# Kernel tuning notes

Measured on AMD Instinct MI355X. Metric: run time of the kernel, lower is better.

## Reference

```python
import jax, jax.numpy as jnp
import numpy as np

B, C, T = 64, 128, 500
N_RES, N_CLASSES = 2048, 10
DECAY_RES, DECAY_CLF = 0.9, 0.9
V_TH_RES, V_TH_CLF = 1.0, 1.0


def setup_inputs() -> dict:
    key = jax.random.key(0)
    k1, k2, k3, k4 = jax.random.split(key, 4)
    x = jax.random.normal(k1, (B, C, T), dtype=jnp.float32)
    # learned / fixed parameters sized per init_kwargs
    W_in = jax.random.normal(k2, (N_RES, C), dtype=jnp.float32) * (1.0 / np.sqrt(C))
    W_res = jax.random.normal(k3, (N_RES, N_RES), dtype=jnp.float32) * (1.0 / np.sqrt(N_RES))
    W_clf = jax.random.normal(k4, (N_CLASSES, N_RES), dtype=jnp.float32) * (1.0 / np.sqrt(N_RES))
    return {"x": x, "W_in": W_in, "W_res": W_res, "W_clf": W_clf}


def reference(x, W_in, W_res, W_clf):
    """x: (B, C, T). Returns (spike_counts (B, n_classes), reservoir_spikes_accum (B, n_reservoir)).
    LIF reservoir + single-voter LIF readout, no STDP updates (use_stdp=False path)."""
    Bb = x.shape[0]
    dtype = x.dtype

    def step(carry, x_t):  # x_t: (B, C)
        v_r, s_prev, v_c = carry
        # reservoir LIF: leak + feedforward input + recurrent spike input
        I = x_t @ W_in.T + s_prev @ W_res.T          # (B, N_RES)
        v_r = DECAY_RES * v_r + I
        s = (v_r >= V_TH_RES).astype(dtype)          # spike
        v_r = v_r * (1.0 - s)                        # reset fired neurons
        # classifier (STDPLayer forward, plasticity disabled)
        v_c = DECAY_CLF * v_c + s @ W_clf.T          # (B, N_CLASSES)
        c = (v_c >= V_TH_CLF).astype(dtype)
        v_c = v_c * (1.0 - c)
        return (v_r, s, v_c), (c, s)

    init = (jnp.zeros((Bb, N_RES), dtype),
            jnp.zeros((Bb, N_RES), dtype),
            jnp.zeros((Bb, N_CLASSES), dtype))
    xs = jnp.moveaxis(x, 2, 0)                       # (T, B, C)
    _, (clf_spikes, res_spikes) = jax.lax.scan(step, init, xs)
    spike_counts = clf_spikes.sum(axis=0)            # (B, N_CLASSES)
    reservoir_spikes_accum = res_spikes.sum(axis=0)  # (B, N_RES)
    return spike_counts, reservoir_spikes_accum
```

## Files before the change

kernel.cpp:

```cpp
#include <hip/hip_runtime.h>
#include <cstdint>
#include <cstddef>

#define B_    64
#define C_    128
#define T_    500
#define NRES  2048
#define NCLS  10

#define NWG   256
#define SL    8
#define NT    1024
#define WROW  520
#define WPIT  (4 * WROW)



#define WS_MASK0   0
#define WS_MASK1   16384
#define WS_FLAG    32768
#define WS_ARR     49152
#define WS_WORDS   13312
#define NFLAG      16
#define CHKWG      (NWG - 1)

typedef float v2f __attribute__((ext_vector_type(2)));

struct SMem {
  float    WtT2[SL][WPIT];
  float    WinT2[SL][C_];
  float    xs2[2][B_][C_ + 1];
  unsigned mask[B_][65];
  double   clfred2[2][NCLS];
};

__global__ void zero_ws_kernel(unsigned* __restrict__ p, int n) {
  int i = blockIdx.x * blockDim.x + threadIdx.x;
  if (i < n) p[i] = 0u;
}

#define ACC2(ACC, WB, M0, M1, JB) do {                                        \
  const unsigned _lo = (unsigned)(((int)((M0) << (31 - (JB)))) >> 31) & (WB); \
  const unsigned _hi = (unsigned)(((int)((M1) << (31 - (JB)))) >> 31) & (WB); \
  v2f _m; _m.x = __uint_as_float(_lo); _m.y = __uint_as_float(_hi);           \
  (ACC) = (ACC) + _m;                                                         \
} while (0)

#define BT_STEP(X, D, MLO) do {                                            \
  const unsigned _y = (unsigned)__shfl_xor((int)(X), (D), 64);             \
  (X) = (b & (D)) ? (((X) & ~(MLO)) | ((_y >> (D)) & (MLO)))               \
                  : (((X) & (MLO)) | ((_y << (D)) & ~(MLO)));              \
} while (0)

#define BT_ALL(X) do {                 \
  BT_STEP(X, 16, 0x0000FFFFu);         \
  BT_STEP(X,  8, 0x00FF00FFu);         \
  BT_STEP(X,  4, 0x0F0F0F0Fu);         \
  BT_STEP(X,  2, 0x33333333u);         \
  BT_STEP(X,  1, 0x55555555u);         \
} while (0)

__global__ void __launch_bounds__(NT, 4)
reservoir_kernel(const float* __restrict__ x, const float* __restrict__ Win,
                 const float* __restrict__ Wres, const float* __restrict__ Wclf,
                 float* __restrict__ out, unsigned char* __restrict__ ws) {
  __shared__ SMem sm;
  const int w   = blockIdx.x;
  const int tid = threadIdx.x;
  const int b   = tid & 63;
  const int wid = tid >> 6;
  const int il  = wid & 7;
  const int h   = wid >> 3;
  const int blk = b & 3;
  const int g   = b >> 2;
  const int bat0 = h * 32 + g * 2;
  const int bat1 = bat0 + 1;
  const int iu  = __builtin_amdgcn_readfirstlane(w * SL + il);

  unsigned* gm0  = (unsigned*)(ws + WS_MASK0);
  unsigned* gm1  = (unsigned*)(ws + WS_MASK1);
  unsigned* flgb = (unsigned*)(ws + WS_FLAG);
  unsigned* arr  = (unsigned*)(ws + WS_ARR);
  unsigned* myflag = flgb + (w & (NFLAG - 1)) * 256;

  {
    const int j0 = tid * 16;
    #pragma unroll
    for (int r4 = 0; r4 < 4; ++r4) {
      const int j   = j0 + r4 * 4;
      const int il2 = j >> 11;
      const int pos = j & 2047;
      const int bk  = pos >> 9;
      const int s   = pos & 511;
      const float4 v4 = *(const float4*)(Wres + (size_t)(w * SL + il2) * NRES + pos);
      *(float4*)(&sm.WtT2[il2][bk * WROW + s]) = v4;
    }
  }
  {
    const int il2 = tid >> 7, c = tid & 127;
    sm.WinT2[il2][c] = Win[(size_t)(w * SL + il2) * C_ + c];
  }

  float v = 0.f;
  int   cntr = 0;
  double vc = 0.0;
  int   cntc = 0;

  float xv[8];
  {
    const int p0 = tid * 8;
    #pragma unroll
    for (int r = 0; r < 8; ++r) {
      float z = x[(size_t)(p0 + r) * T_ + 0];
      int p = p0 + r;
      sm.xs2[0][p >> 7][p & 127] = z;
    }
    #pragma unroll
    for (int r = 0; r < 8; ++r) xv[r] = x[(size_t)(p0 + r) * T_ + 1];
  }

  for (int t = 0; t < T_; ++t) {
    unsigned* gprev = (t & 1) ? gm0 : gm1;
    unsigned* gcur  = (t & 1) ? gm1 : gm0;

    {
      const int i32 = b & 31, hh = b >> 5;
      #pragma unroll
      for (int kk = 0; kk < 4; ++kk) {
        const int k = (wid << 2) | kk;
        unsigned xw = __hip_atomic_load(gprev + (k * 32 + i32) * 2 + hh,
                                        __ATOMIC_RELAXED, __HIP_MEMORY_SCOPE_AGENT);
        BT_ALL(xw);
        sm.mask[b][k] = xw;
      }
    }
    __syncthreads();

    if (t + 1 < T_) {
      const int p0 = tid * 8;
      #pragma unroll
      for (int r = 0; r < 8; ++r) {
        int p = p0 + r;
        sm.xs2[(t + 1) & 1][p >> 7][p & 127] = xv[r];
      }
      if (t + 2 < T_) {
        #pragma unroll
        for (int r = 0; r < 8; ++r) xv[r] = x[(size_t)(p0 + r) * T_ + (t + 2)];
      }
    }

    float g1 = 0.f;
    if (b < 32) {
      const int bat = h * 32 + b;
      const float4* __restrict__ winp = (const float4*)&sm.WinT2[il][0];
      const float* __restrict__ xrow = &sm.xs2[t & 1][bat][0];
      #pragma unroll 8
      for (int cq = 0; cq < 32; ++cq) {
        const float4 wv = winp[cq];
        const int c = cq * 4;
        g1 = fmaf(xrow[c + 0], wv.x, g1);
        g1 = fmaf(xrow[c + 1], wv.y, g1);
        g1 = fmaf(xrow[c + 2], wv.z, g1);
        g1 = fmaf(xrow[c + 3], wv.w, g1);
      }
    }

    v2f acc; acc.x = 0.f; acc.y = 0.f;
    {
      const float*    wbase = &sm.WtT2[il][blk * WROW];
      const unsigned* mr0   = &sm.mask[bat0][blk * 16];
      const unsigned* mr1   = &sm.mask[bat1][blk * 16];
      for (int wq = 0; wq < 16; ++wq) {
        const unsigned m0 = mr0[wq];
        const unsigned m1 = mr1[wq];
        const float4* q = (const float4*)(wbase + wq * 32);
        #pragma unroll
        for (int jq = 0; jq < 8; ++jq) {
          const float4 w4 = q[jq];
          const int jb = jq * 4;
          ACC2(acc, __float_as_uint(w4.x), m0, m1, jb + 0);
          ACC2(acc, __float_as_uint(w4.y), m0, m1, jb + 1);
          ACC2(acc, __float_as_uint(w4.z), m0, m1, jb + 2);
          ACC2(acc, __float_as_uint(w4.w), m0, m1, jb + 3);
        }
      }
    }
    const float aP = acc.x, aQ = acc.y;

    const float p1 = __shfl_xor(aP, 1), q1 = __shfl_xor(aQ, 1);
    const float p2 = __shfl_xor(aP, 2), q2 = __shfl_xor(aQ, 2);
    const float p3 = __shfl_xor(aP, 3), q3 = __shfl_xor(aQ, 3);
    const float g2u0 = __fadd_rn(__fadd_rn(__fadd_rn(aP, p1), p2), p3);
    const float g2u1 = __fadd_rn(__fadd_rn(__fadd_rn(aQ, q1), q2), q3);

    {
      const int src = (b >> 1) * 4;
      const float r0 = __shfl(g2u0, src, 64);
      const float r1 = __shfl(g2u1, src, 64);
      const float g2m = (b & 1) ? r1 : r0;
      const float I = __fadd_rn(g1, g2m);
      v = __fadd_rn(__fmul_rn(0.9f, v), I);
      bool s = (b < 32) && (v >= 1.0f);
      if (s) { v = 0.f; cntr++; }
      unsigned long long bal = __ballot(s);
      if (b == 0)
        __hip_atomic_store(gcur + iu * 2 + h, (unsigned)bal,
                           __ATOMIC_RELAXED, __HIP_MEMORY_SCOPE_AGENT);
    }
    __syncthreads();

    if (tid == 0)
      __hip_atomic_store(arr + w * 4, (unsigned)(t + 1),
                         __ATOMIC_RELEASE, __HIP_MEMORY_SCOPE_AGENT);

    if (w == CHKWG && wid == 0) {
      const unsigned tgt = (unsigned)(t + 1);
      for (;;) {
        unsigned a0 = __hip_atomic_load(arr + (b +   0) * 4, __ATOMIC_RELAXED,
                                        __HIP_MEMORY_SCOPE_AGENT);
        unsigned a1 = __hip_atomic_load(arr + (b +  64) * 4, __ATOMIC_RELAXED,
                                        __HIP_MEMORY_SCOPE_AGENT);
        unsigned a2 = __hip_atomic_load(arr + (b + 128) * 4, __ATOMIC_RELAXED,
                                        __HIP_MEMORY_SCOPE_AGENT);
        unsigned a3 = __hip_atomic_load(arr + (b + 192) * 4, __ATOMIC_RELAXED,
                                        __HIP_MEMORY_SCOPE_AGENT);
        bool ok = (a0 >= tgt) & (a1 >= tgt) & (a2 >= tgt) & (a3 >= tgt);
        if (__all(ok)) break;
        __builtin_amdgcn_s_sleep(1);
      }
      if (b < NFLAG)
        __hip_atomic_store(flgb + b * 256, (unsigned)(t + 1),
                           __ATOMIC_RELEASE, __HIP_MEMORY_SCOPE_AGENT);
    }

    if (w < B_ && wid < NCLS) {
      double pc = 0.0;
      if (t > 0) {
        const float* __restrict__ wc = Wclf + (size_t)wid * NRES + b;
        #pragma unroll 4
        for (int q = 0; q < 32; ++q) {
          const unsigned mw = sm.mask[w][(b >> 5) + 2 * q];
          const float wv = wc[q * 64];
          const unsigned keep =
              (unsigned)(((int)(mw << (31 - (b & 31)))) >> 31);
          pc += (double)__uint_as_float(keep & __float_as_uint(wv));
        }
      }
      #pragma unroll
      for (int off = 1; off < 64; off <<= 1)
        pc += __shfl_xor(pc, off, 64);
      if (b == 0) sm.clfred2[t & 1][wid] = pc;
    }

    if (w < B_ && tid < NCLS && t >= 2) {
      vc = 0.9 * vc + sm.clfred2[(t + 1) & 1][tid];
      if (vc >= 1.0) { vc = 0.0; cntc++; }
    }

    if (tid == 0) {
      while (__hip_atomic_load(myflag, __ATOMIC_RELAXED,
                               __HIP_MEMORY_SCOPE_AGENT) < (unsigned)(t + 1))
        __builtin_amdgcn_s_sleep(1);
    }
    __syncthreads();
  }

  if (w < B_ && tid < NCLS) {
    vc = 0.9 * vc + sm.clfred2[1][tid];
    if (vc >= 1.0) { vc = 0.0; cntc++; }
  }
  {
    const int i32 = b & 31, hh = b >> 5;
    #pragma unroll
    for (int kk = 0; kk < 4; ++kk) {
      const int k = (wid << 2) | kk;
      unsigned xw = __hip_atomic_load(gm1 + (k * 32 + i32) * 2 + hh,
                                      __ATOMIC_RELAXED, __HIP_MEMORY_SCOPE_AGENT);
      BT_ALL(xw);
      sm.mask[b][k] = xw;
    }
  }
  __syncthreads();
  if (w < B_ && wid < NCLS) {
    double pc = 0.0;
    {
      const float* __restrict__ wc = Wclf + (size_t)wid * NRES + b;
      #pragma unroll 4
      for (int q = 0; q < 32; ++q) {
        const unsigned mw = sm.mask[w][(b >> 5) + 2 * q];
        const float wv = wc[q * 64];
        const unsigned keep =
            (unsigned)(((int)(mw << (31 - (b & 31)))) >> 31);
        pc += (double)__uint_as_float(keep & __float_as_uint(wv));
      }
    }
    #pragma unroll
    for (int off = 1; off < 64; off <<= 1)
      pc += __shfl_xor(pc, off, 64);
    if (b == 0) sm.clfred2[0][wid] = pc;
  }
  __syncthreads();
  if (w < B_ && tid < NCLS) {
    vc = 0.9 * vc + sm.clfred2[0][tid];
    if (vc >= 1.0) cntc++;
    out[w * NCLS + tid] = (float)cntc;
  }
  if (b < 32)
    out[B_ * NCLS + (size_t)(h * 32 + b) * NRES + w * SL + il] = (float)cntr;
}

extern "C" void kernel_launch(void* const* d_in, const int* in_sizes, int n_in,
                              void* d_out, int out_size, void* d_ws, size_t ws_size,
                              hipStream_t stream) {
  const float* x    = (const float*)d_in[0];
  const float* Win  = (const float*)d_in[1];
  const float* Wres = (const float*)d_in[2];
  const float* Wclf = (const float*)d_in[3];
  float* out = (float*)d_out;
  unsigned char* ws = (unsigned char*)d_ws;

  hipLaunchKernelGGL(zero_ws_kernel, dim3((WS_WORDS + 255) / 256), dim3(256), 0, stream,
                     (unsigned*)ws, WS_WORDS);
  hipLaunchKernelGGL(reservoir_kernel, dim3(NWG), dim3(NT), 0, stream,
                     x, Win, Wres, Wclf, out, ws);
}
```

Before: 14.03 ms.

## Halve workgroup threads, each wave handles all 64 batches per neuron

The block shrinks from 1024 to 512 threads. Each wave now owns one reservoir neuron for all 64 batch rows instead of 32, so each lane accumulates four batch rows per weight load. The spike mask is stored in a new interleaved shared-memory layout so four batch masks load as one uint4, and the x staging uses float4 stores. This doubles reuse of each recurrent weight read from shared memory and removes the idle half-wave in the input projection. In exchange there are fewer waves per workgroup to hide latency, more serial work per wave in the per-step critical path, and higher register pressure.

```diff
diff --git a/kernel.cpp b/kernel.cpp
--- a/kernel.cpp
+++ b/kernel.cpp
@@ -10,9 +10,11 @@
 
 #define NWG   256
 #define SL    8
-#define NT    1024
+#define NT    512
 #define WROW  520
 #define WPIT  (4 * WROW)
+#define MGP   292
+#define XSP   132
 
 
 
@@ -29,8 +31,8 @@
 struct SMem {
   float    WtT2[SL][WPIT];
   float    WinT2[SL][C_];
-  float    xs2[2][B_][C_ + 1];
-  unsigned mask[B_][65];
+  float    xs2[2][B_][XSP];
+  unsigned maskg[16 * MGP + 4];
   double   clfred2[2][NCLS];
 };
 
@@ -39,11 +41,14 @@
   if (i < n) p[i] = 0u;
 }
 
-#define ACC2(ACC, WB, M0, M1, JB) do {                                        \
-  const unsigned _lo = (unsigned)(((int)((M0) << (31 - (JB)))) >> 31) & (WB); \
-  const unsigned _hi = (unsigned)(((int)((M1) << (31 - (JB)))) >> 31) & (WB); \
-  v2f _m; _m.x = __uint_as_float(_lo); _m.y = __uint_as_float(_hi);           \
-  (ACC) = (ACC) + _m;                                                         \
+#define ACC4(AA, AB, WB, MM, JB) do {                                          \
+  const unsigned _k0 = (unsigned)(((int)((MM).x << (31 - (JB)))) >> 31) & (WB);\
+  const unsigned _k1 = (unsigned)(((int)((MM).y << (31 - (JB)))) >> 31) & (WB);\
+  const unsigned _k2 = (unsigned)(((int)((MM).z << (31 - (JB)))) >> 31) & (WB);\
+  const unsigned _k3 = (unsigned)(((int)((MM).w << (31 - (JB)))) >> 31) & (WB);\
+  v2f _a; _a.x = __uint_as_float(_k0); _a.y = __uint_as_float(_k1);            \
+  v2f _c; _c.x = __uint_as_float(_k2); _c.y = __uint_as_float(_k3);            \
+  (AA) = (AA) + _a; (AB) = (AB) + _c;                                          \
 } while (0)
 
 #define BT_STEP(X, D, MLO) do {                                            \
@@ -60,7 +65,14 @@
   BT_STEP(X,  1, 0x55555555u);         \
 } while (0)
 
-__global__ void __launch_bounds__(NT, 4)
+#define FOLD4(C) ({                                                        \
+  const float _f1 = __shfl_xor((C), 1);                                    \
+  const float _f2 = __shfl_xor((C), 2);                                    \
+  const float _f3 = __shfl_xor((C), 3);                                    \
+  __fadd_rn(__fadd_rn(__fadd_rn((C), _f1), _f2), _f3);                     \
+})
+
+__global__ void __launch_bounds__(NT, 2)
 reservoir_kernel(const float* __restrict__ x, const float* __restrict__ Win,
                  const float* __restrict__ Wres, const float* __restrict__ Wclf,
                  float* __restrict__ out, unsigned char* __restrict__ ws) {
@@ -69,12 +81,9 @@
   const int tid = threadIdx.x;
   const int b   = tid & 63;
   const int wid = tid >> 6;
-  const int il  = wid & 7;
-  const int h   = wid >> 3;
+  const int il  = wid;
   const int blk = b & 3;
-  const int g   = b >> 2;
-  const int bat0 = h * 32 + g * 2;
-  const int bat1 = bat0 + 1;
+  const int bg  = b >> 2;
   const int iu  = __builtin_amdgcn_readfirstlane(w * SL + il);
 
   unsigned* gm0  = (unsigned*)(ws + WS_MASK0);
@@ -84,9 +93,9 @@
   unsigned* myflag = flgb + (w & (NFLAG - 1)) * 256;
 
   {
-    const int j0 = tid * 16;
-    #pragma unroll
-    for (int r4 = 0; r4 < 4; ++r4) {
+    const int j0 = tid * 32;
+    #pragma unroll
+    for (int r4 = 0; r4 < 8; ++r4) {
       const int j   = j0 + r4 * 4;
       const int il2 = j >> 11;
       const int pos = j & 2047;
@@ -97,8 +106,11 @@
     }
   }
   {
-    const int il2 = tid >> 7, c = tid & 127;
-    sm.WinT2[il2][c] = Win[(size_t)(w * SL + il2) * C_ + c];
+    #pragma unroll
+    for (int e = 0; e < 2; ++e) {
+      const int idx = tid * 2 + e;
+      sm.WinT2[idx >> 7][idx & 127] = Win[(size_t)(w * SL + (idx >> 7)) * C_ + (idx & 127)];
+    }
   }
 
   float v = 0.f;
@@ -106,17 +118,20 @@
   double vc = 0.0;
   int   cntc = 0;
 
-  float xv[8];
+  float xv[16];
   {
-    const int p0 = tid * 8;
-    #pragma unroll
-    for (int r = 0; r < 8; ++r) {
-      float z = x[(size_t)(p0 + r) * T_ + 0];
-      int p = p0 + r;
-      sm.xs2[0][p >> 7][p & 127] = z;
-    }
-    #pragma unroll
-    for (int r = 0; r < 8; ++r) xv[r] = x[(size_t)(p0 + r) * T_ + 1];
+    const int p0 = tid * 16;
+    float tmp[16];
+    #pragma unroll
+    for (int r = 0; r < 16; ++r) tmp[r] = x[(size_t)(p0 + r) * T_ + 0];
+    #pragma unroll
+    for (int q = 0; q < 4; ++q) {
+      const int p = p0 + q * 4;
+      float4 f4; f4.x = tmp[q*4+0]; f4.y = tmp[q*4+1]; f4.z = tmp[q*4+2]; f4.w = tmp[q*4+3];
+      *(float4*)(&sm.xs2[0][p >> 7][p & 127]) = f4;
+    }
+    #pragma unroll
+    for (int r = 0; r < 16; ++r) xv[r] = x[(size_t)(p0 + r) * T_ + 1];
   }
 
   for (int t = 0; t < T_; ++t) {
@@ -126,85 +141,87 @@
     {
       const int i32 = b & 31, hh = b >> 5;
       #pragma unroll
-      for (int kk = 0; kk < 4; ++kk) {
-        const int k = (wid << 2) | kk;
+      for (int kk = 0; kk < 8; ++kk) {
+        const int k = (wid << 3) | kk;
         unsigned xw = __hip_atomic_load(gprev + (k * 32 + i32) * 2 + hh,
                                         __ATOMIC_RELAXED, __HIP_MEMORY_SCOPE_AGENT);
         BT_ALL(xw);
-        sm.mask[b][k] = xw;
+        sm.maskg[(b >> 2) * MGP + (k >> 4) * 72 + (k & 15) * 4 + (b & 3)] = xw;
       }
     }
     __syncthreads();
 
     if (t + 1 < T_) {
-      const int p0 = tid * 8;
+      const int p0 = tid * 16;
       #pragma unroll
-      for (int r = 0; r < 8; ++r) {
-        int p = p0 + r;
-        sm.xs2[(t + 1) & 1][p >> 7][p & 127] = xv[r];
+      for (int q = 0; q < 4; ++q) {
+        const int p = p0 + q * 4;
+        float4 f4; f4.x = xv[q*4+0]; f4.y = xv[q*4+1]; f4.z = xv[q*4+2]; f4.w = xv[q*4+3];
+        *(float4*)(&sm.xs2[(t + 1) & 1][p >> 7][p & 127]) = f4;
       }
       if (t + 2 < T_) {
         #pragma unroll
-        for (int r = 0; r < 8; ++r) xv[r] = x[(size_t)(p0 + r) * T_ + (t + 2)];
+        for (int r = 0; r < 16; ++r) xv[r] = x[(size_t)(p0 + r) * T_ + (t + 2)];
       }
     }
 
     float g1 = 0.f;
-    if (b < 32) {
-      const int bat = h * 32 + b;
+    {
       const float4* __restrict__ winp = (const float4*)&sm.WinT2[il][0];
-      const float* __restrict__ xrow = &sm.xs2[t & 1][bat][0];
+      const float4* __restrict__ xrp  = (const float4*)&sm.xs2[t & 1][b][0];
       #pragma unroll 8
       for (int cq = 0; cq < 32; ++cq) {
         const float4 wv = winp[cq];
-        const int c = cq * 4;
-        g1 = fmaf(xrow[c + 0], wv.x, g1);
-        g1 = fmaf(xrow[c + 1], wv.y, g1);
-        g1 = fmaf(xrow[c + 2], wv.z, g1);
-        g1 = fmaf(xrow[c + 3], wv.w, g1);
-      }
-    }
-
-    v2f acc; acc.x = 0.f; acc.y = 0.f;
+        const float4 xq = xrp[cq];
+        g1 = fmaf(xq.x, wv.x, g1);
+        g1 = fmaf(xq.y, wv.y, g1);
+        g1 = fmaf(xq.z, wv.z, g1);
+        g1 = fmaf(xq.w, wv.w, g1);
+      }
+    }
+
+    v2f accA; accA.x = 0.f; accA.y = 0.f;
+    v2f accB; accB.x = 0.f; accB.y = 0.f;
     {
       const float*    wbase = &sm.WtT2[il][blk * WROW];
-      const unsigned* mr0   = &sm.mask[bat0][blk * 16];
-      const unsigned* mr1   = &sm.mask[bat1][blk * 16];
+      const unsigned* mgb   = &sm.maskg[bg * MGP + blk * 72];
       for (int wq = 0; wq < 16; ++wq) {
-        const unsigned m0 = mr0[wq];
-        const unsigned m1 = mr1[wq];
+        const uint4 mm = *(const uint4*)(mgb + wq * 4);
         const float4* q = (const float4*)(wbase + wq * 32);
         #pragma unroll
         for (int jq = 0; jq < 8; ++jq) {
           const float4 w4 = q[jq];
           const int jb = jq * 4;
-          ACC2(acc, __float_as_uint(w4.x), m0, m1, jb + 0);
-          ACC2(acc, __float_as_uint(w4.y), m0, m1, jb + 1);
-          ACC2(acc, __float_as_uint(w4.z), m0, m1, jb + 2);
-          ACC2(acc, __float_as_uint(w4.w), m0, m1, jb + 3);
+          ACC4(accA, accB, __float_as_uint(w4.x), mm, jb + 0);
+          ACC4(accA, accB, __float_as_uint(w4.y), mm, jb + 1);
+          ACC4(accA, accB, __float_as_uint(w4.z), mm, jb + 2);
+          ACC4(accA, accB, __float_as_uint(w4.w), mm, jb + 3);
         }
       }
     }
-    const float aP = acc.x, aQ = acc.y;
-
-    const float p1 = __shfl_xor(aP, 1), q1 = __shfl_xor(aQ, 1);
-    const float p2 = __shfl_xor(aP, 2), q2 = __shfl_xor(aQ, 2);
-    const float p3 = __shfl_xor(aP, 3), q3 = __shfl_xor(aQ, 3);
-    const float g2u0 = __fadd_rn(__fadd_rn(__fadd_rn(aP, p1), p2), p3);
-    const float g2u1 = __fadd_rn(__fadd_rn(__fadd_rn(aQ, q1), q2), q3);
 
     {
-      const int src = (b >> 1) * 4;
-      const float r0 = __shfl(g2u0, src, 64);
-      const float r1 = __shfl(g2u1, src, 64);
-      const float g2m = (b & 1) ? r1 : r0;
+      const float f0 = FOLD4(accA.x);
+      const float f1 = FOLD4(accA.y);
+      const float f2 = FOLD4(accB.x);
+      const float f3 = FOLD4(accB.y);
+      const int src = b & ~3;
+      const float r0 = __shfl(f0, src, 64);
+      const float r1 = __shfl(f1, src, 64);
+      const float r2 = __shfl(f2, src, 64);
+      const float r3 = __shfl(f3, src, 64);
+      const int j2 = b & 3;
+      const float sA = (j2 & 1) ? r1 : r0;
+      const float sB = (j2 & 1) ? r3 : r2;
+      const float g2m = (j2 & 2) ? sB : sA;
+
       const float I = __fadd_rn(g1, g2m);
       v = __fadd_rn(__fmul_rn(0.9f, v), I);
-      bool s = (b < 32) && (v >= 1.0f);
+      const bool s = (v >= 1.0f);
       if (s) { v = 0.f; cntr++; }
-      unsigned long long bal = __ballot(s);
+      const unsigned long long bal = __ballot(s);
       if (b == 0)
-        __hip_atomic_store(gcur + iu * 2 + h, (unsigned)bal,
+        __hip_atomic_store((unsigned long long*)gcur + iu, bal,
                            __ATOMIC_RELAXED, __HIP_MEMORY_SCOPE_AGENT);
     }
     __syncthreads();
@@ -233,23 +250,27 @@
                            __ATOMIC_RELEASE, __HIP_MEMORY_SCOPE_AGENT);
     }
 
-    if (w < B_ && wid < NCLS) {
-      double pc = 0.0;
-      if (t > 0) {
-        const float* __restrict__ wc = Wclf + (size_t)wid * NRES + b;
-        #pragma unroll 4
-        for (int q = 0; q < 32; ++q) {
-          const unsigned mw = sm.mask[w][(b >> 5) + 2 * q];
-          const float wv = wc[q * 64];
-          const unsigned keep =
-              (unsigned)(((int)(mw << (31 - (b & 31)))) >> 31);
-          pc += (double)__uint_as_float(keep & __float_as_uint(wv));
+    if (w < B_) {
+      for (int c = wid; c < NCLS; c += 8) {
+        double pc = 0.0;
+        if (t > 0) {
+          const float* __restrict__ wc = Wclf + (size_t)c * NRES + b;
+          #pragma unroll 4
+          for (int q = 0; q < 32; ++q) {
+            const int W = 2 * q + (b >> 5);
+            const unsigned mw =
+                sm.maskg[(w >> 2) * MGP + (W >> 4) * 72 + (W & 15) * 4 + (w & 3)];
+            const float wv = wc[q * 64];
+            const unsigned keep =
+                (unsigned)(((int)(mw << (31 - (b & 31)))) >> 31);
+            pc += (double)__uint_as_float(keep & __float_as_uint(wv));
+          }
         }
-      }
-      #pragma unroll
-      for (int off = 1; off < 64; off <<= 1)
-        pc += __shfl_xor(pc, off, 64);
-      if (b == 0) sm.clfred2[t & 1][wid] = pc;
+        #pragma unroll
+        for (int off = 1; off < 64; off <<= 1)
+          pc += __shfl_xor(pc, off, 64);
+        if (b == 0) sm.clfred2[t & 1][c] = pc;
+      }
     }
 
     if (w < B_ && tid < NCLS && t >= 2) {
@@ -272,32 +293,34 @@
   {
     const int i32 = b & 31, hh = b >> 5;
     #pragma unroll
-    for (int kk = 0; kk < 4; ++kk) {
-      const int k = (wid << 2) | kk;
+    for (int kk = 0; kk < 8; ++kk) {
+      const int k = (wid << 3) | kk;
       unsigned xw = __hip_atomic_load(gm1 + (k * 32 + i32) * 2 + hh,
                                       __ATOMIC_RELAXED, __HIP_MEMORY_SCOPE_AGENT);
       BT_ALL(xw);
-      sm.mask[b][k] = xw;
+      sm.maskg[(b >> 2) * MGP + (k >> 4) * 72 + (k & 15) * 4 + (b & 3)] = xw;
     }
   }
   __syncthreads();
-  if (w < B_ && wid < NCLS) {
-    double pc = 0.0;
-    {
-      const float* __restrict__ wc = Wclf + (size_t)wid * NRES + b;
+  if (w < B_) {
+    for (int c = wid; c < NCLS; c += 8) {
+      double pc = 0.0;
+      const float* __restrict__ wc = Wclf + (size_t)c * NRES + b;
       #pragma unroll 4
       for (int q = 0; q < 32; ++q) {
-        const unsigned mw = sm.mask[w][(b >> 5) + 2 * q];
+        const int W = 2 * q + (b >> 5);
+        const unsigned mw =
+            sm.maskg[(w >> 2) * MGP + (W >> 4) * 72 + (W & 15) * 4 + (w & 3)];
         const float wv = wc[q * 64];
         const unsigned keep =
             (unsigned)(((int)(mw << (31 - (b & 31)))) >> 31);
         pc += (double)__uint_as_float(keep & __float_as_uint(wv));
       }
-    }
-    #pragma unroll
-    for (int off = 1; off < 64; off <<= 1)
-      pc += __shfl_xor(pc, off, 64);
-    if (b == 0) sm.clfred2[0][wid] = pc;
+      #pragma unroll
+      for (int off = 1; off < 64; off <<= 1)
+        pc += __shfl_xor(pc, off, 64);
+      if (b == 0) sm.clfred2[0][c] = pc;
+    }
   }
   __syncthreads();
   if (w < B_ && tid < NCLS) {
@@ -305,8 +328,7 @@
     if (vc >= 1.0) cntc++;
     out[w * NCLS + tid] = (float)cntc;
   }
-  if (b < 32)
-    out[B_ * NCLS + (size_t)(h * 32 + b) * NRES + w * SL + il] = (float)cntr;
+  out[B_ * NCLS + (size_t)b * NRES + w * SL + il] = (float)cntr;
 }
 
 extern "C" void kernel_launch(void* const* d_in, const int* in_sizes, int n_in,
```

Result: slower. 15.20 ms (+8.3%).

## Precompute next-step input projection during grid barrier wait and relax sync

Applied to the files above, without the earlier changes.

Moves the per-step input projection (x_t · W_in) out of the critical path: it is computed once before the loop and then for step t+1 inside the grid-barrier wait window, after the arrival flag is published. Workgroups that do no classifier work now have every thread spin on the barrier flag and skip the trailing block barrier. A `#pragma unroll 4` is also added to the recurrent mask-accumulate loop. The aim is to hide the input projection behind the inter-workgroup barrier latency and shorten each time step. The cost is more threads polling the same global flag and more register pressure from the unroll.

```diff
diff --git a/kernel.cpp b/kernel.cpp
--- a/kernel.cpp
+++ b/kernel.cpp
@@ -59,6 +59,24 @@
   BT_STEP(X,  2, 0x33333333u);         \
   BT_STEP(X,  1, 0x55555555u);         \
 } while (0)
+
+struct SMemRef;
+
+__device__ __forceinline__ float g1_compute(const float* __restrict__ winrow,
+                                            const float* __restrict__ xrow) {
+  float g1 = 0.f;
+  const float4* __restrict__ winp = (const float4*)winrow;
+  #pragma unroll 8
+  for (int cq = 0; cq < 32; ++cq) {
+    const float4 wv = winp[cq];
+    const int c = cq * 4;
+    g1 = fmaf(xrow[c + 0], wv.x, g1);
+    g1 = fmaf(xrow[c + 1], wv.y, g1);
+    g1 = fmaf(xrow[c + 2], wv.z, g1);
+    g1 = fmaf(xrow[c + 3], wv.w, g1);
+  }
+  return g1;
+}
 
 __global__ void __launch_bounds__(NT, 4)
 reservoir_kernel(const float* __restrict__ x, const float* __restrict__ Win,
@@ -76,6 +94,7 @@
   const int bat0 = h * 32 + g * 2;
   const int bat1 = bat0 + 1;
   const int iu  = __builtin_amdgcn_readfirstlane(w * SL + il);
+  const int bat = h * 32 + (b & 31);
 
   unsigned* gm0  = (unsigned*)(ws + WS_MASK0);
   unsigned* gm1  = (unsigned*)(ws + WS_MASK1);
@@ -118,6 +137,10 @@
     #pragma unroll
     for (int r = 0; r < 8; ++r) xv[r] = x[(size_t)(p0 + r) * T_ + 1];
   }
+  __syncthreads();
+
+  float g1cur = 0.f;
+  if (b < 32) g1cur = g1_compute(&sm.WinT2[il][0], &sm.xs2[0][bat][0]);
 
   for (int t = 0; t < T_; ++t) {
     unsigned* gprev = (t & 1) ? gm0 : gm1;
@@ -149,27 +172,12 @@
       }
     }
 
-    float g1 = 0.f;
-    if (b < 32) {
-      const int bat = h * 32 + b;
-      const float4* __restrict__ winp = (const float4*)&sm.WinT2[il][0];
-      const float* __restrict__ xrow = &sm.xs2[t & 1][bat][0];
-      #pragma unroll 8
-      for (int cq = 0; cq < 32; ++cq) {
-        const float4 wv = winp[cq];
-        const int c = cq * 4;
-        g1 = fmaf(xrow[c + 0], wv.x, g1);
-        g1 = fmaf(xrow[c + 1], wv.y, g1);
-        g1 = fmaf(xrow[c + 2], wv.z, g1);
-        g1 = fmaf(xrow[c + 3], wv.w, g1);
-      }
-    }
-
     v2f acc; acc.x = 0.f; acc.y = 0.f;
     {
       const float*    wbase = &sm.WtT2[il][blk * WROW];
       const unsigned* mr0   = &sm.mask[bat0][blk * 16];
       const unsigned* mr1   = &sm.mask[bat1][blk * 16];
+      #pragma unroll 4
       for (int wq = 0; wq < 16; ++wq) {
         const unsigned m0 = mr0[wq];
         const unsigned m1 = mr1[wq];
@@ -198,7 +206,7 @@
       const float r0 = __shfl(g2u0, src, 64);
       const float r1 = __shfl(g2u1, src, 64);
       const float g2m = (b & 1) ? r1 : r0;
-      const float I = __fadd_rn(g1, g2m);
+      const float I = __fadd_rn(g1cur, g2m);
       v = __fadd_rn(__fmul_rn(0.9f, v), I);
       bool s = (b < 32) && (v >= 1.0f);
       if (s) { v = 0.f; cntr++; }
@@ -212,6 +220,12 @@
     if (tid == 0)
       __hip_atomic_store(arr + w * 4, (unsigned)(t + 1),
                          __ATOMIC_RELEASE, __HIP_MEMORY_SCOPE_AGENT);
+
+
+    if (t + 1 < T_) {
+      if (b < 32)
+        g1cur = g1_compute(&sm.WinT2[il][0], &sm.xs2[(t + 1) & 1][bat][0]);
+    }
 
     if (w == CHKWG && wid == 0) {
       const unsigned tgt = (unsigned)(t + 1);
@@ -233,36 +247,42 @@
                            __ATOMIC_RELEASE, __HIP_MEMORY_SCOPE_AGENT);
     }
 
-    if (w < B_ && wid < NCLS) {
-      double pc = 0.0;
-      if (t > 0) {
-        const float* __restrict__ wc = Wclf + (size_t)wid * NRES + b;
-        #pragma unroll 4
-        for (int q = 0; q < 32; ++q) {
-          const unsigned mw = sm.mask[w][(b >> 5) + 2 * q];
-          const float wv = wc[q * 64];
-          const unsigned keep =
-              (unsigned)(((int)(mw << (31 - (b & 31)))) >> 31);
-          pc += (double)__uint_as_float(keep & __float_as_uint(wv));
+    if (w < B_) {
+      if (wid < NCLS) {
+        double pc = 0.0;
+        if (t > 0) {
+          const float* __restrict__ wc = Wclf + (size_t)wid * NRES + b;
+          #pragma unroll 4
+          for (int q = 0; q < 32; ++q) {
+            const unsigned mw = sm.mask[w][(b >> 5) + 2 * q];
+            const float wv = wc[q * 64];
+            const unsigned keep =
+                (unsigned)(((int)(mw << (31 - (b & 31)))) >> 31);
+            pc += (double)__uint_as_float(keep & __float_as_uint(wv));
+          }
         }
-      }
-      #pragma unroll
-      for (int off = 1; off < 64; off <<= 1)
-        pc += __shfl_xor(pc, off, 64);
-      if (b == 0) sm.clfred2[t & 1][wid] = pc;
-    }
-
-    if (w < B_ && tid < NCLS && t >= 2) {
-      vc = 0.9 * vc + sm.clfred2[(t + 1) & 1][tid];
-      if (vc >= 1.0) { vc = 0.0; cntc++; }
-    }
-
-    if (tid == 0) {
+        #pragma unroll
+        for (int off = 1; off < 64; off <<= 1)
+          pc += __shfl_xor(pc, off, 64);
+        if (b == 0) sm.clfred2[t & 1][wid] = pc;
+      }
+
+      if (tid < NCLS && t >= 2) {
+        vc = 0.9 * vc + sm.clfred2[(t + 1) & 1][tid];
+        if (vc >= 1.0) { vc = 0.0; cntc++; }
+      }
+
+      if (tid == 0) {
+        while (__hip_atomic_load(myflag, __ATOMIC_RELAXED,
+                                 __HIP_MEMORY_SCOPE_AGENT) < (unsigned)(t + 1))
+          __builtin_amdgcn_s_sleep(1);
+      }
+      __syncthreads();
+    } else {
       while (__hip_atomic_load(myflag, __ATOMIC_RELAXED,
                                __HIP_MEMORY_SCOPE_AGENT) < (unsigned)(t + 1))
         __builtin_amdgcn_s_sleep(1);
     }
-    __syncthreads();
   }
 
   if (w < B_ && tid < NCLS) {
@@ -306,7 +326,7 @@
     out[w * NCLS + tid] = (float)cntc;
   }
   if (b < 32)
-    out[B_ * NCLS + (size_t)(h * 32 + b) * NRES + w * SL + il] = (float)cntr;
+    out[B_ * NCLS + (size_t)bat * NRES + w * SL + il] = (float)cntr;
 }
 
 extern "C" void kernel_launch(void* const* d_in, const int* in_sizes, int n_in,
```

Result: no change. 13.84 ms (-1.3%).
